# Optimization experiments

Measured on AMD Instinct MI355X. Metric: run time of the kernel, lower is better.

Reference implementation:

```python
import jax, jax.numpy as jnp
import numpy as np

DIM = 768
H = 12
D = DIM // H  # head_dim = 64
SCALE = D ** -0.5


def _split_heads(x):
    # [b, n, h*d] -> [b, h, n, d]
    b, n, _ = x.shape
    return x.reshape(b, n, H, D).transpose(0, 2, 1, 3)


def setup_inputs() -> dict:
    key = jax.random.key(0)
    ks = jax.random.split(key, 16)
    B, NQ, NKV = 2, 2048, 2048
    w_init = lambda k: jax.random.normal(k, (DIM, DIM), dtype=jnp.float32) * 0.02
    return {
        "words": jax.random.normal(ks[0], (B, NQ, DIM), dtype=jnp.float32),
        "position_words": jax.random.normal(ks[1], (B, NQ, DIM), dtype=jnp.float32),
        "conscious_words": jax.random.normal(ks[2], (B, NQ, DIM), dtype=jnp.float32),
        "cross_kv": jax.random.normal(ks[3], (B, NKV, DIM), dtype=jnp.float32),
        "position_cross": jax.random.normal(ks[4], (B, NKV, DIM), dtype=jnp.float32),
        "Wq_w": w_init(ks[5]), "Wk_w": w_init(ks[6]), "Wv_w": w_init(ks[7]),
        "Wq_p": w_init(ks[8]), "Wk_p": w_init(ks[9]),
        "Wq_c": w_init(ks[10]), "Wk_c": w_init(ks[11]),
        "latent_k": jax.random.normal(ks[12], (DIM,), dtype=jnp.float32),
        "Wo": w_init(ks[13]),
        "bo": jnp.zeros((DIM,), dtype=jnp.float32),
    }


def reference(words, position_words, conscious_words, cross_kv, position_cross,
              Wq_w, Wk_w, Wv_w, Wq_p, Wk_p, Wq_c, Wk_c, latent_k, Wo, bo):
    # Queries from three sources. Sum of the 9 pairwise QK^T scores equals
    # (sum of Qs) @ (sum of Ks)^T by bilinearity of matmul (same math as source).
    q = _split_heads(words @ Wq_w) + _split_heads(position_words @ Wq_p) \
        + _split_heads(conscious_words @ Wq_c)        # [b,h,nq,d]
    # latent conscious key: same vector for every kv position
    kc = (latent_k @ Wk_c).reshape(H, D)              # [h,d]
    k = _split_heads(cross_kv @ Wk_w) + _split_heads(position_cross @ Wk_p) \
        + kc[None, :, None, :]                        # [b,h,nkv,d]
    v = _split_heads(cross_kv @ Wv_w)                 # [b,h,nkv,d]

    score = jnp.einsum('bhid,bhjd->bhij', q, k) * SCALE  # [b,h,nq,nkv]
    attn = jax.nn.softmax(score, axis=-1)
    out = jnp.einsum('bhij,bhjd->bhid', attn, v)      # [b,h,nq,d]
    b, _, nq, _ = out.shape
    out = out.transpose(0, 2, 1, 3).reshape(b, nq, H * D)
    return out @ Wo + bo
```

## Files before the change

### kernel.cpp

```cpp
#include <hip/hip_runtime.h>
#include <math.h>

#define DIM  768
#define NH   12
#define HD   64
#define NQ   2048
#define NKV  2048
#define QSC_LOG2E 0.18033688011112042f

typedef short bf16x8  __attribute__((ext_vector_type(8)));
typedef float f32x4   __attribute__((ext_vector_type(4)));
typedef float f32x16  __attribute__((ext_vector_type(16)));

__device__ __forceinline__ unsigned short f2bf(float f) {
    unsigned u = __float_as_uint(f);
    unsigned r = (u + 0x7FFFu + ((u >> 16) & 1u)) >> 16;
    return (unsigned short)r;
}
__device__ __forceinline__ float bf2f(unsigned short u) {
    return __uint_as_float(((unsigned)u) << 16);
}

__device__ __forceinline__ unsigned cvtpk_bf16(float a, float b) {
    unsigned r;
    asm("v_cvt_pk_bf16_f32 %0, %1, %2" : "=v"(r) : "v"(a), "v"(b));
    return r;
}

__device__ __forceinline__ void plswap(unsigned& a, unsigned& b) {
    asm("v_permlane32_swap_b32 %0, %1" : "+v"(a), "+v"(b));
}

__device__ __forceinline__ float vexp2f(float x) {
#if __has_builtin(__builtin_amdgcn_exp2f)
    return __builtin_amdgcn_exp2f(x);
#else
    float r;
    asm("v_exp_f32 %0, %1\ns_nop 0" : "=v"(r) : "v"(x));
    return r;
#endif
}

__device__ __forceinline__ void ld_lds16(void* lds, const void* g) {
    __builtin_amdgcn_global_load_lds(
        (const __attribute__((address_space(1))) unsigned int*)g,
        (__attribute__((address_space(3))) unsigned int*)lds, 16, 0, 0);
}

__device__ __forceinline__ f32x16 z16() {
    f32x16 r;
    #pragma unroll
    for (int e = 0; e < 16; ++e) r[e] = 0.f;
    return r;
}

union PB16 { unsigned u[4]; bf16x8 v; };

__global__ __launch_bounds__(256)
void prep_kernel(const float* __restrict__ w0, const float* __restrict__ w1,
                 const float* __restrict__ w2, const float* __restrict__ w3,
                 const float* __restrict__ w4, const float* __restrict__ w5,
                 const float* __restrict__ w6, unsigned short* __restrict__ wt,
                 const float* __restrict__ latent, const float* __restrict__ Wkc,
                 float* __restrict__ kc) {
    __shared__ float t[32][33];
    int bid = blockIdx.x;
    if (bid < 4032) {
        int iz = bid / 576, rem = bid - iz * 576;
        int iy = rem / 24, ix = rem - iy * 24;
        const float* Ws[7] = {w0, w1, w2, w3, w4, w5, w6};
        const float* W = Ws[iz];
        unsigned short* D = wt + (size_t)iz * (768 * 768);
        int r0 = iy * 32, c0 = ix * 32;
        int tx = threadIdx.x & 31, ty = threadIdx.x >> 5;
        #pragma unroll
        for (int yy = 0; yy < 4; ++yy)
            t[ty * 4 + yy][tx] = W[(size_t)(r0 + ty * 4 + yy) * 768 + c0 + tx];
        __syncthreads();
        #pragma unroll
        for (int yy = 0; yy < 4; ++yy)
            D[(size_t)(c0 + ty * 4 + yy) * 768 + r0 + tx] = f2bf(t[tx][ty * 4 + yy]);
    } else {
        int jb = bid - 4032;
        float (&red)[16][17] = *reinterpret_cast<float(*)[16][17]>(&t[0][0]);
        int tx = threadIdx.x & 15, ty = threadIdx.x >> 4;
        int j = jb * 16 + tx;
        float acc = 0.f;
        for (int i = ty * 48; i < ty * 48 + 48; ++i)
            acc += latent[i] * Wkc[i * DIM + j];
        red[ty][tx] = acc;
        __syncthreads();
        if (ty == 0) {
            float s = 0.f;
            #pragma unroll
            for (int k = 0; k < 16; ++k) s += red[k][tx];
            kc[j] = s;
        }
    }
}

struct QCfg {
    const float* A0; const float* A1; const float* A2;
    const unsigned short* B0; const unsigned short* B1; const unsigned short* B2;
    const float* bias; float scale; void* out; int npair; int mode;
};

__global__ __launch_bounds__(256, 3)
void gemm_qvk(QCfg c0, QCfg c1, QCfg c2) {
    __shared__ unsigned short As[2][64 * 64];
    __shared__ unsigned short Bs[2][128 * 64];
    const int tid = threadIdx.x;
    const int w = tid >> 6, l = tid & 63, g = l >> 4, r16 = l & 15;

    int p = blockIdx.x;
    int xcd = p & 7, s = p >> 3;
    int bx = s % 6, gg = s / 6;
    int gidx = gg * 8 + xcd;
    int by = gidx & 63, z = gidx >> 6;
    const int n0 = bx * 128, m0 = by * 64;

    QCfg c = (z == 0) ? c0 : (z == 1) ? c1 : c2;
    const float* Alist[3] = {c.A0, c.A1, c.A2};
    const unsigned short* Blist[3] = {c.B0, c.B1, c.B2};

    const int ar = tid >> 2, ac = (tid & 3) * 16;
    const int aswz = (ar & 7) << 4;

    f32x4 acc[4][2];
    #pragma unroll
    for (int i = 0; i < 4; ++i)
        #pragma unroll
        for (int j = 0; j < 2; ++j) acc[i][j] = (f32x4){0.f, 0.f, 0.f, 0.f};

    const int NSTEPS = c.npair * 12;
    int pnA = 0, knA = 0;
    int pnB = 0, knB = 0;
    float4 xa0, xa1, xa2, xa3;
    float4 ya0, ya1, ya2, ya3;

#define ALOADX { const float* _ap = Alist[pnA] + (size_t)(m0 + ar) * 768 + knA + ac; \
    xa0 = *(const float4*)_ap;       xa1 = *(const float4*)(_ap + 4); \
    xa2 = *(const float4*)(_ap + 8); xa3 = *(const float4*)(_ap + 12); \
    knA += 64; if (knA == 768) { knA = 0; ++pnA; } }
#define ALOADY { const float* _ap = Alist[pnA] + (size_t)(m0 + ar) * 768 + knA + ac; \
    ya0 = *(const float4*)_ap;       ya1 = *(const float4*)(_ap + 4); \
    ya2 = *(const float4*)(_ap + 8); ya3 = *(const float4*)(_ap + 12); \
    knA += 64; if (knA == 768) { knA = 0; ++pnA; } }
#define AWR(BUFI, v0, v1, v2, v3) { uint4 u0_, u1_; \
    u0_.x = cvtpk_bf16(v0.x, v0.y); u0_.y = cvtpk_bf16(v0.z, v0.w); \
    u0_.z = cvtpk_bf16(v1.x, v1.y); u0_.w = cvtpk_bf16(v1.z, v1.w); \
    u1_.x = cvtpk_bf16(v2.x, v2.y); u1_.y = cvtpk_bf16(v2.z, v2.w); \
    u1_.z = cvtpk_bf16(v3.x, v3.y); u1_.w = cvtpk_bf16(v3.z, v3.w); \
    char* _dst = (char*)As[BUFI] + ar * 128; \
    *(uint4*)(_dst + ((2 * ac) ^ aswz)) = u0_; \
    *(uint4*)(_dst + ((2 * ac + 16) ^ aswz)) = u1_; }
#define BSTG(BUFI) { const unsigned short* _bp = Blist[pnB]; \
    _Pragma("unroll") \
    for (int is = 0; is < 4; ++is) { \
        int u = is * 256 + tid, r = u >> 3, cc2 = u & 7; \
        int col = ((cc2 ^ (r & 7)) << 3); \
        ld_lds16((char*)Bs[BUFI] + is * 4096 + w * 1024, \
                 _bp + (size_t)(n0 + r) * 768 + knB + col); } \
    knB += 64; if (knB == 768) { knB = 0; ++pnB; } }
#define COMPUTE(BUFI) { const char* Ab = (const char*)As[BUFI]; \
    const char* Bb = (const char*)Bs[BUFI]; \
    _Pragma("unroll") \
    for (int kk = 0; kk < 2; ++kk) { \
        bf16x8 af[4], bf[2]; \
        _Pragma("unroll") \
        for (int i = 0; i < 4; ++i) { int row = i * 16 + r16; \
            af[i] = *(const bf16x8*)(Ab + row * 128 + ((kk * 64 + g * 16) ^ ((row & 7) << 4))); } \
        _Pragma("unroll") \
        for (int j = 0; j < 2; ++j) { int row = w * 32 + j * 16 + r16; \
            bf[j] = *(const bf16x8*)(Bb + row * 128 + ((kk * 64 + g * 16) ^ ((row & 7) << 4))); } \
        _Pragma("unroll") \
        for (int i = 0; i < 4; ++i) \
            _Pragma("unroll") \
            for (int j = 0; j < 2; ++j) \
                acc[i][j] = __builtin_amdgcn_mfma_f32_16x16x32_bf16( \
                    af[i], bf[j], acc[i][j], 0, 0, 0); } }
#define WAITV4 asm volatile("s_waitcnt vmcnt(4)" ::: "memory")
#define WAITV0 asm volatile("s_waitcnt vmcnt(0)" ::: "memory")
#define WAITL0 asm volatile("s_waitcnt lgkmcnt(0)" ::: "memory")

    ALOADX;
    BSTG(0);
    ALOADY;
    AWR(0, xa0, xa1, xa2, xa3);
    WAITV4; WAITL0;
    __builtin_amdgcn_s_barrier();

    const int P = NSTEPS >> 1;
    #pragma unroll 1
    for (int it = 0; it < P; ++it) {
        const int st = it * 2;
        BSTG(1);
        const bool a2 = (st + 2 < NSTEPS);
        if (a2) ALOADX;
        COMPUTE(0);
        AWR(1, ya0, ya1, ya2, ya3);
        if (a2) { WAITV4; } else { WAITV0; }
        WAITL0;
        __builtin_amdgcn_s_barrier();
        const bool b2 = (st + 2 < NSTEPS);
        const bool a3 = (st + 3 < NSTEPS);
        if (b2) BSTG(0);
        if (a3) ALOADY;
        COMPUTE(1);
        if (b2) {
            AWR(0, xa0, xa1, xa2, xa3);
            if (a3) { WAITV4; } else { WAITV0; }
            WAITL0;
            __builtin_amdgcn_s_barrier();
        }
    }
#undef ALOADX
#undef ALOADY
#undef AWR
#undef BSTG
#undef COMPUTE
#undef WAITV4
#undef WAITV0
#undef WAITL0

    const int mode = c.mode;
    #pragma unroll
    for (int i = 0; i < 4; ++i) {
        #pragma unroll
        for (int j = 0; j < 2; ++j) {
            int col = n0 + w * 32 + j * 16 + r16;
            float bv = (mode == 0 && c.bias) ? c.bias[col] : 0.f;
            #pragma unroll
            for (int rr = 0; rr < 4; ++rr) {
                int row = m0 + i * 16 + g * 4 + rr;
                float v = acc[i][j][rr];
                if (mode == 2) v *= c.scale;
                v += bv;
                if (mode == 3) {
                    int bb = row >> 11, q = row & 2047;
                    ((unsigned short*)c.out)[(size_t)(bb * 768 + col) * 2048 + q] = f2bf(v);
                } else {
                    ((unsigned short*)c.out)[(size_t)row * 768 + col] = f2bf(v);
                }
            }
        }
    }
}

__global__ __launch_bounds__(256)
void gemm_out(const unsigned short* __restrict__ A,
              const unsigned short* __restrict__ B,
              const float* __restrict__ bias, float* __restrict__ Cout) {
    __shared__ unsigned short As[2][64 * 64];
    __shared__ unsigned short Bs[2][128 * 64];
    const int tid = threadIdx.x;
    const int w = tid >> 6, l = tid & 63, g = l >> 4, r16 = l & 15;

    int o_lin = blockIdx.x;
    int wl = (o_lin & 7) * 48 + (o_lin >> 3);
    int bx = wl % 6, by = wl / 6;
    const int n0 = bx * 128, m0 = by * 64;

    f32x4 acc[4][2];
    #pragma unroll
    for (int i = 0; i < 4; ++i)
        #pragma unroll
        for (int j = 0; j < 2; ++j) acc[i][j] = (f32x4){0.f, 0.f, 0.f, 0.f};

#define GSTAGE(BUFI, K0) { \
    _Pragma("unroll") \
    for (int is = 0; is < 2; ++is) { \
        int u = is * 256 + tid, r = u >> 3, cc = u & 7; \
        int col = ((cc ^ (r & 7)) << 3); \
        ld_lds16((char*)As[BUFI] + is * 4096 + w * 1024, \
                 A + (size_t)(m0 + r) * 768 + (K0) + col); } \
    _Pragma("unroll") \
    for (int is = 0; is < 4; ++is) { \
        int u = is * 256 + tid, r = u >> 3, cc = u & 7; \
        int col = ((cc ^ (r & 7)) << 3); \
        ld_lds16((char*)Bs[BUFI] + is * 4096 + w * 1024, \
                 B + (size_t)(n0 + r) * 768 + (K0) + col); } }

    GSTAGE(0, 0);
    __syncthreads();

    #pragma unroll 1
    for (int st = 0; st < 12; ++st) {
        int cur = st & 1;
        if (st + 1 < 12) GSTAGE(cur ^ 1, (st + 1) * 64);
        const char* Ab = (const char*)As[cur];
        const char* Bb = (const char*)Bs[cur];
        #pragma unroll
        for (int kk = 0; kk < 2; ++kk) {
            bf16x8 af[4], bf[2];
            #pragma unroll
            for (int i = 0; i < 4; ++i) {
                int row = i * 16 + r16;
                af[i] = *(const bf16x8*)(Ab + row * 128 +
                          ((kk * 64 + g * 16) ^ ((row & 7) << 4)));
            }
            #pragma unroll
            for (int j = 0; j < 2; ++j) {
                int row = w * 32 + j * 16 + r16;
                bf[j] = *(const bf16x8*)(Bb + row * 128 +
                          ((kk * 64 + g * 16) ^ ((row & 7) << 4)));
            }
            #pragma unroll
            for (int i = 0; i < 4; ++i)
                #pragma unroll
                for (int j = 0; j < 2; ++j)
                    acc[i][j] = __builtin_amdgcn_mfma_f32_16x16x32_bf16(
                        af[i], bf[j], acc[i][j], 0, 0, 0);
        }
        __syncthreads();
    }
#undef GSTAGE

    #pragma unroll
    for (int i = 0; i < 4; ++i) {
        #pragma unroll
        for (int j = 0; j < 2; ++j) {
            int col = n0 + w * 32 + j * 16 + r16;
            float bv = bias[col];
            #pragma unroll
            for (int rr = 0; rr < 4; ++rr) {
                int row = m0 + i * 16 + g * 4 + rr;
                Cout[(size_t)row * 768 + col] = acc[i][j][rr] + bv;
            }
        }
    }
}

__global__ __launch_bounds__(256)
void flash2(const unsigned short* __restrict__ Qb,
            const unsigned short* __restrict__ Kb,
            const unsigned short* __restrict__ Vt,
            unsigned short* __restrict__ P0, unsigned short* __restrict__ P1,
            unsigned short* __restrict__ P2, unsigned short* __restrict__ P3,
            float2* __restrict__ ML) {
    __shared__ unsigned short KV[2][2][4096];
    const int tid = threadIdx.x;
    const int w = tid >> 6, l = tid & 63, lo = l & 31, hi = l >> 5;

    int p = blockIdx.x + 64 * blockIdx.y;
    int xcd = p & 7, s = p >> 3;
    int gg = s >> 6, inner = s & 63;
    int bh = gg * 8 + xcd;
    int qi = inner >> 2, part = inner & 3;
    int b = bh / NH, h = bh % NH;
    int q0 = qi * 128;
    int kvbase = part * 512;

    bf16x8 qf[4];
    {
        const unsigned short* Qrow =
            Qb + (size_t)(b * NQ + q0 + w * 32 + lo) * DIM + h * HD + hi * 8;
        #pragma unroll
        for (int kc = 0; kc < 4; ++kc) qf[kc] = *(const bf16x8*)(Qrow + kc * 16);
    }

    f32x16 o0 = z16(), o1 = z16();
    float m = -3.0e38f, lsum = 0.f;

    const unsigned short* Kbase = Kb + (size_t)(b * NKV) * DIM + h * HD;
    const unsigned short* Vbase = Vt + ((size_t)b * DIM + h * HD) * NKV;

#define FSTAGE(BUFI, T0) { \
    _Pragma("unroll") \
    for (int is = 0; is < 2; ++is) { \
        int u = is * 256 + tid, r = u >> 3, cc = u & 7; \
        int col = ((cc ^ (r & 7)) << 3); \
        ld_lds16((char*)KV[BUFI][0] + is * 4096 + w * 1024, \
                 Kbase + (size_t)((T0) + r) * 768 + col); \
        ld_lds16((char*)KV[BUFI][1] + is * 4096 + w * 1024, \
                 Vbase + (size_t)r * 2048 + (T0) + col); } }

    FSTAGE(0, kvbase);
    __syncthreads();

    #pragma unroll 1
    for (int t = 0; t < 8; ++t) {
        int cur = t & 1;
        if (t < 7) FSTAGE(cur ^ 1, kvbase + (t + 1) * 64);

        const char* Kp = (const char*)KV[cur][0];
        const char* Vp = (const char*)KV[cur][1];

        f32x16 s0 = z16(), s1 = z16();
        __builtin_amdgcn_s_setprio(1);
        #pragma unroll
        for (int kc = 0; kc < 4; ++kc) {
            int r0 = lo, r1 = 32 + lo;
            bf16x8 k0 = *(const bf16x8*)(Kp + r0 * 128 +
                          ((kc * 32 + hi * 16) ^ ((r0 & 7) << 4)));
            bf16x8 k1 = *(const bf16x8*)(Kp + r1 * 128 +
                          ((kc * 32 + hi * 16) ^ ((r1 & 7) << 4)));
            s0 = __builtin_amdgcn_mfma_f32_32x32x16_bf16(k0, qf[kc], s0, 0, 0, 0);
            s1 = __builtin_amdgcn_mfma_f32_32x32x16_bf16(k1, qf[kc], s1, 0, 0, 0);
        }
        __builtin_amdgcn_s_setprio(0);

        float a8[8];
        #pragma unroll
        for (int e = 0; e < 8; ++e)
            a8[e] = fmaxf(fmaxf(fmaxf(s0[e], s0[e + 8]), s1[e]), s1[e + 8]);
        float pm = fmaxf(fmaxf(fmaxf(a8[0], a8[1]), fmaxf(a8[2], a8[3])),
                         fmaxf(fmaxf(a8[4], a8[5]), fmaxf(a8[6], a8[7])));
        pm = fmaxf(pm, __shfl_xor(pm, 32));

        if (__any(pm > m + 10.f)) {
            float mn = fmaxf(m, pm);
            float sc = vexp2f(m - mn);
            lsum *= sc;
            #pragma unroll
            for (int e = 0; e < 16; ++e) { o0[e] *= sc; o1[e] *= sc; }
            m = mn;
        }

        #pragma unroll
        for (int e = 0; e < 16; ++e) {
            s0[e] = vexp2f(s0[e] - m);
            s1[e] = vexp2f(s1[e] - m);
        }

        float b8[8];
        #pragma unroll
        for (int e = 0; e < 8; ++e)
            b8[e] = (s0[e] + s0[e + 8]) + (s1[e] + s1[e + 8]);
        float rs = ((b8[0] + b8[1]) + (b8[2] + b8[3])) +
                   ((b8[4] + b8[5]) + (b8[6] + b8[7]));
        rs += __shfl_xor(rs, 32);
        lsum += rs;

        PB16 pb[4];
        #pragma unroll
        for (int cc = 0; cc < 2; ++cc) {
            unsigned a0 = cvtpk_bf16(s0[cc * 8 + 0], s0[cc * 8 + 1]);
            unsigned a1 = cvtpk_bf16(s0[cc * 8 + 2], s0[cc * 8 + 3]);
            unsigned b0 = cvtpk_bf16(s0[cc * 8 + 4], s0[cc * 8 + 5]);
            unsigned b1 = cvtpk_bf16(s0[cc * 8 + 6], s0[cc * 8 + 7]);
            plswap(a0, b0);
            plswap(a1, b1);
            pb[cc].u[0] = a0; pb[cc].u[1] = a1; pb[cc].u[2] = b0; pb[cc].u[3] = b1;
            unsigned c0 = cvtpk_bf16(s1[cc * 8 + 0], s1[cc * 8 + 1]);
            unsigned c1 = cvtpk_bf16(s1[cc * 8 + 2], s1[cc * 8 + 3]);
            unsigned d0 = cvtpk_bf16(s1[cc * 8 + 4], s1[cc * 8 + 5]);
            unsigned d1 = cvtpk_bf16(s1[cc * 8 + 6], s1[cc * 8 + 7]);
            plswap(c0, d0);
            plswap(c1, d1);
            pb[2 + cc].u[0] = c0; pb[2 + cc].u[1] = c1;
            pb[2 + cc].u[2] = d0; pb[2 + cc].u[3] = d1;
        }

        __builtin_amdgcn_s_setprio(1);
        #pragma unroll
        for (int c = 0; c < 4; ++c) {
            int r0 = lo, r1 = 32 + lo;
            bf16x8 v0 = *(const bf16x8*)(Vp + r0 * 128 +
                          ((c * 32 + hi * 16) ^ ((r0 & 7) << 4)));
            bf16x8 v1 = *(const bf16x8*)(Vp + r1 * 128 +
                          ((c * 32 + hi * 16) ^ ((r1 & 7) << 4)));
            o0 = __builtin_amdgcn_mfma_f32_32x32x16_bf16(v0, pb[c].v, o0, 0, 0, 0);
            o1 = __builtin_amdgcn_mfma_f32_32x32x16_bf16(v1, pb[c].v, o1, 0, 0, 0);
        }
        __builtin_amdgcn_s_setprio(0);
        __syncthreads();
    }
#undef FSTAGE

    unsigned short* Pp = (part == 0) ? P0 : (part == 1) ? P1 : (part == 2) ? P2 : P3;
    const int q = q0 + w * 32 + lo;
    unsigned short* Op = Pp + ((size_t)bh * 2048 + q) * 64;
    #pragma unroll
    for (int grp = 0; grp < 4; ++grp) {
        int r0 = grp * 4;
        int d0 = grp * 8 + 4 * hi;
        uint2 v0, v1;
        v0.x = cvtpk_bf16(o0[r0 + 0], o0[r0 + 1]);
        v0.y = cvtpk_bf16(o0[r0 + 2], o0[r0 + 3]);
        *(uint2*)(Op + d0) = v0;
        v1.x = cvtpk_bf16(o1[r0 + 0], o1[r0 + 1]);
        v1.y = cvtpk_bf16(o1[r0 + 2], o1[r0 + 3]);
        *(uint2*)(Op + 32 + d0) = v1;
    }
    if (hi == 0)
        ML[(size_t)(part * 24 + bh) * 2048 + q] = make_float2(m, lsum);
}

__global__ __launch_bounds__(256)
void combine4(const unsigned short* __restrict__ P0, const unsigned short* __restrict__ P1,
              const unsigned short* __restrict__ P2, const unsigned short* __restrict__ P3,
              const float2* __restrict__ ML, unsigned short* __restrict__ AO) {
    int bh = blockIdx.y;
    int idx = blockIdx.x * 256 + threadIdx.x;
    int q = idx >> 1, dh = (idx & 1) * 32;

    float2 u0 = ML[(size_t)(0 * 24 + bh) * 2048 + q];
    float2 u1 = ML[(size_t)(1 * 24 + bh) * 2048 + q];
    float2 u2 = ML[(size_t)(2 * 24 + bh) * 2048 + q];
    float2 u3 = ML[(size_t)(3 * 24 + bh) * 2048 + q];
    float M = fmaxf(fmaxf(u0.x, u1.x), fmaxf(u2.x, u3.x));
    float w0 = vexp2f(u0.x - M), w1 = vexp2f(u1.x - M);
    float w2 = vexp2f(u2.x - M), w3 = vexp2f(u3.x - M);
    float inv = 1.f / (w0 * u0.y + w1 * u1.y + w2 * u2.y + w3 * u3.y);
    w0 *= inv; w1 *= inv; w2 *= inv; w3 *= inv;

    size_t off = ((size_t)bh * 2048 + q) * 64 + dh;
    float acc[32];
    #pragma unroll
    for (int e = 0; e < 32; ++e) acc[e] = 0.f;
    const unsigned short* Ps[4] = {P0, P1, P2, P3};
    float ws[4] = {w0, w1, w2, w3};
    #pragma unroll
    for (int pp = 0; pp < 4; ++pp) {
        const unsigned short* src = Ps[pp] + off;
        float wv = ws[pp];
        #pragma unroll
        for (int c = 0; c < 4; ++c) {
            uint4 vv = *(const uint4*)(src + c * 8);
            unsigned uu[4] = {vv.x, vv.y, vv.z, vv.w};
            #pragma unroll
            for (int e = 0; e < 4; ++e) {
                acc[c * 8 + e * 2 + 0] += wv * bf2f((unsigned short)(uu[e] & 0xFFFF));
                acc[c * 8 + e * 2 + 1] += wv * bf2f((unsigned short)(uu[e] >> 16));
            }
        }
    }
    int b = bh / NH, h = bh % NH;
    unsigned short* dst = AO + ((size_t)(b * 2048 + q)) * DIM + h * HD + dh;
    #pragma unroll
    for (int c = 0; c < 4; ++c) {
        uint4 ov;
        ov.x = cvtpk_bf16(acc[c * 8 + 0], acc[c * 8 + 1]);
        ov.y = cvtpk_bf16(acc[c * 8 + 2], acc[c * 8 + 3]);
        ov.z = cvtpk_bf16(acc[c * 8 + 4], acc[c * 8 + 5]);
        ov.w = cvtpk_bf16(acc[c * 8 + 6], acc[c * 8 + 7]);
        *(uint4*)(dst + c * 8) = ov;
    }
}

extern "C" void kernel_launch(void* const* d_in, const int* in_sizes, int n_in,
                              void* d_out, int out_size, void* d_ws, size_t ws_size,
                              hipStream_t stream) {
    const float* words   = (const float*)d_in[0];
    const float* posw    = (const float*)d_in[1];
    const float* consc   = (const float*)d_in[2];
    const float* cross   = (const float*)d_in[3];
    const float* pcross  = (const float*)d_in[4];
    const float* Wq_w    = (const float*)d_in[5];
    const float* Wk_w    = (const float*)d_in[6];
    const float* Wv_w    = (const float*)d_in[7];
    const float* Wq_p    = (const float*)d_in[8];
    const float* Wk_p    = (const float*)d_in[9];
    const float* Wq_c    = (const float*)d_in[10];
    const float* Wk_c    = (const float*)d_in[11];
    const float* latentk = (const float*)d_in[12];
    const float* Wo      = (const float*)d_in[13];
    const float* bo      = (const float*)d_in[14];

    char* arena = (char*)d_ws;
    const size_t WTE = 768 * 768;
    unsigned short* WT = (unsigned short*)(arena);
    unsigned short* QB = (unsigned short*)(arena + 8257536);
    unsigned short* VT = (unsigned short*)(arena + 14548992);
    unsigned short* KB = (unsigned short*)(arena + 20840448);
    unsigned short* P0 = (unsigned short*)(arena + 27131904);
    unsigned short* P1 = (unsigned short*)(arena + 33423360);
    unsigned short* P2 = (unsigned short*)(arena + 39714816);
    unsigned short* P3 = (unsigned short*)(arena);
    float2* ML         = (float2*)(arena + 46006272);
    float* KCV         = (float*)(arena + 47579136);

    prep_kernel<<<dim3(4080), dim3(256), 0, stream>>>(
        Wq_w, Wq_p, Wq_c, Wk_w, Wk_p, Wv_w, Wo, WT, latentk, Wk_c, KCV);

    QCfg cq = { words, posw, consc,
                WT + 0 * WTE, WT + 1 * WTE, WT + 2 * WTE,
                nullptr, QSC_LOG2E, QB, 3, 2 };
    QCfg cv = { cross, nullptr, nullptr,
                WT + 5 * WTE, nullptr, nullptr,
                nullptr, 1.f, VT, 1, 3 };
    QCfg ck = { cross, pcross, nullptr,
                WT + 3 * WTE, WT + 4 * WTE, nullptr,
                KCV, 1.f, KB, 2, 0 };
    gemm_qvk<<<dim3(1152), dim3(256), 0, stream>>>(cq, cv, ck);

    flash2<<<dim3(64, 24), dim3(256), 0, stream>>>(QB, KB, VT, P0, P1, P2, P3, ML);

    combine4<<<dim3(16, 24), dim3(256), 0, stream>>>(P0, P1, P2, P3, ML, QB);

    gemm_out<<<dim3(384), dim3(256), 0, stream>>>(QB, WT + 6 * WTE, bo, (float*)d_out);
}
```

Baseline: 142.1 us.

## Deepen QKV projection GEMM pipeline to triple-buffered LDS stages

Converts the projection GEMM's double-buffered LDS pipeline into a three-stage ring. A and B tiles are prefetched two steps ahead, with vmcnt waits retuned for the deeper queue, so global load latency is hidden behind more compute. The cost is more LDS per block (three buffers) and more live A registers. The launch bound minimum of 3 blocks per SM is also dropped, which can reduce occupancy.

```diff
diff --git a/kernel.cpp b/kernel.cpp
--- a/kernel.cpp
+++ b/kernel.cpp
@@ -105,10 +105,10 @@
     const float* bias; float scale; void* out; int npair; int mode;
 };
 
-__global__ __launch_bounds__(256, 3)
+__global__ __launch_bounds__(256)
 void gemm_qvk(QCfg c0, QCfg c1, QCfg c2) {
-    __shared__ unsigned short As[2][64 * 64];
-    __shared__ unsigned short Bs[2][128 * 64];
+    __shared__ unsigned short As[3][64 * 64];
+    __shared__ unsigned short Bs[3][128 * 64];
     const int tid = threadIdx.x;
     const int w = tid >> 6, l = tid & 63, g = l >> 4, r16 = l & 15;
 
@@ -137,14 +137,12 @@
     int pnB = 0, knB = 0;
     float4 xa0, xa1, xa2, xa3;
     float4 ya0, ya1, ya2, ya3;
-
-#define ALOADX { const float* _ap = Alist[pnA] + (size_t)(m0 + ar) * 768 + knA + ac; \
-    xa0 = *(const float4*)_ap;       xa1 = *(const float4*)(_ap + 4); \
-    xa2 = *(const float4*)(_ap + 8); xa3 = *(const float4*)(_ap + 12); \
-    knA += 64; if (knA == 768) { knA = 0; ++pnA; } }
-#define ALOADY { const float* _ap = Alist[pnA] + (size_t)(m0 + ar) * 768 + knA + ac; \
-    ya0 = *(const float4*)_ap;       ya1 = *(const float4*)(_ap + 4); \
-    ya2 = *(const float4*)(_ap + 8); ya3 = *(const float4*)(_ap + 12); \
+    float4 za0, za1, za2, za3;
+
+#define ALOAD(p0, p1, p2, p3) { \
+    const float* _ap = Alist[pnA] + (size_t)(m0 + ar) * 768 + knA + ac; \
+    p0 = *(const float4*)_ap;       p1 = *(const float4*)(_ap + 4); \
+    p2 = *(const float4*)(_ap + 8); p3 = *(const float4*)(_ap + 12); \
     knA += 64; if (knA == 768) { knA = 0; ++pnA; } }
 #define AWR(BUFI, v0, v1, v2, v3) { uint4 u0_, u1_; \
     u0_.x = cvtpk_bf16(v0.x, v0.y); u0_.y = cvtpk_bf16(v0.z, v0.w); \
@@ -179,49 +177,59 @@
             for (int j = 0; j < 2; ++j) \
                 acc[i][j] = __builtin_amdgcn_mfma_f32_16x16x32_bf16( \
                     af[i], bf[j], acc[i][j], 0, 0, 0); } }
+#define WAITV8 asm volatile("s_waitcnt vmcnt(8)" ::: "memory")
 #define WAITV4 asm volatile("s_waitcnt vmcnt(4)" ::: "memory")
 #define WAITV0 asm volatile("s_waitcnt vmcnt(0)" ::: "memory")
 #define WAITL0 asm volatile("s_waitcnt lgkmcnt(0)" ::: "memory")
-
-    ALOADX;
+#define BARRIER __builtin_amdgcn_s_barrier()
+
+    ALOAD(xa0, xa1, xa2, xa3);
+    ALOAD(ya0, ya1, ya2, ya3);
+    ALOAD(za0, za1, za2, za3);
     BSTG(0);
-    ALOADY;
+    BSTG(1);
     AWR(0, xa0, xa1, xa2, xa3);
-    WAITV4; WAITL0;
-    __builtin_amdgcn_s_barrier();
-
-    const int P = NSTEPS >> 1;
+    WAITV4;
+    WAITL0;
+    BARRIER;
+
+    const int NIT = NSTEPS / 3;
     #pragma unroll 1
-    for (int it = 0; it < P; ++it) {
-        const int st = it * 2;
-        BSTG(1);
-        const bool a2 = (st + 2 < NSTEPS);
-        if (a2) ALOADX;
+    for (int it = 0; it < NIT; ++it) {
+        const bool lastit = (it == NIT - 1);
+        if (!lastit) ALOAD(xa0, xa1, xa2, xa3);
+        BSTG(2);
         COMPUTE(0);
         AWR(1, ya0, ya1, ya2, ya3);
-        if (a2) { WAITV4; } else { WAITV0; }
+        if (!lastit) { WAITV8; } else { WAITV4; }
         WAITL0;
-        __builtin_amdgcn_s_barrier();
-        const bool b2 = (st + 2 < NSTEPS);
-        const bool a3 = (st + 3 < NSTEPS);
-        if (b2) BSTG(0);
-        if (a3) ALOADY;
+        BARRIER;
+        if (!lastit) { ALOAD(ya0, ya1, ya2, ya3); BSTG(0); }
         COMPUTE(1);
-        if (b2) {
+        AWR(2, za0, za1, za2, za3);
+        if (!lastit) { WAITV8; } else { WAITV0; }
+        WAITL0;
+        BARRIER;
+        if (!lastit) {
+            ALOAD(za0, za1, za2, za3); BSTG(1);
+            COMPUTE(2);
             AWR(0, xa0, xa1, xa2, xa3);
-            if (a3) { WAITV4; } else { WAITV0; }
+            WAITV8;
             WAITL0;
-            __builtin_amdgcn_s_barrier();
-        }
-    }
-#undef ALOADX
-#undef ALOADY
+            BARRIER;
+        } else {
+            COMPUTE(2);
+        }
+    }
+#undef ALOAD
 #undef AWR
 #undef BSTG
 #undef COMPUTE
+#undef WAITV8
 #undef WAITV4
 #undef WAITV0
 #undef WAITL0
+#undef BARRIER
 
     const int mode = c.mode;
     #pragma unroll
```

Result: slower. 150.1 us (+5.6%).

## Fuse split-KV combine into flash kernel via last-block atomic counter

Applied to the files above, without the earlier changes.

Removes the separate combine4 kernel. Each flash2 block now bumps a per-(head, query-tile) atomic counter after writing its partial output and its max/sum pair. The fourth block to finish merges the four partials into the attention output buffer. This saves one kernel launch and one dependency boundary, at the cost of a memset of the counters, thread fences, and extra serial tail work in the last-arriving block.

```diff
diff --git a/kernel.cpp b/kernel.cpp
--- a/kernel.cpp
+++ b/kernel.cpp
@@ -337,8 +337,10 @@
             const unsigned short* __restrict__ Vt,
             unsigned short* __restrict__ P0, unsigned short* __restrict__ P1,
             unsigned short* __restrict__ P2, unsigned short* __restrict__ P3,
-            float2* __restrict__ ML) {
+            float2* __restrict__ ML, unsigned int* __restrict__ cnt,
+            unsigned short* __restrict__ AO) {
     __shared__ unsigned short KV[2][2][4096];
+    __shared__ int lastFlag;
     const int tid = threadIdx.x;
     const int w = tid >> 6, l = tid & 63, lo = l & 31, hi = l >> 5;
 
@@ -485,57 +487,60 @@
     }
     if (hi == 0)
         ML[(size_t)(part * 24 + bh) * 2048 + q] = make_float2(m, lsum);
-}
-
-__global__ __launch_bounds__(256)
-void combine4(const unsigned short* __restrict__ P0, const unsigned short* __restrict__ P1,
-              const unsigned short* __restrict__ P2, const unsigned short* __restrict__ P3,
-              const float2* __restrict__ ML, unsigned short* __restrict__ AO) {
-    int bh = blockIdx.y;
-    int idx = blockIdx.x * 256 + threadIdx.x;
-    int q = idx >> 1, dh = (idx & 1) * 32;
-
-    float2 u0 = ML[(size_t)(0 * 24 + bh) * 2048 + q];
-    float2 u1 = ML[(size_t)(1 * 24 + bh) * 2048 + q];
-    float2 u2 = ML[(size_t)(2 * 24 + bh) * 2048 + q];
-    float2 u3 = ML[(size_t)(3 * 24 + bh) * 2048 + q];
-    float M = fmaxf(fmaxf(u0.x, u1.x), fmaxf(u2.x, u3.x));
-    float w0 = vexp2f(u0.x - M), w1 = vexp2f(u1.x - M);
-    float w2 = vexp2f(u2.x - M), w3 = vexp2f(u3.x - M);
-    float inv = 1.f / (w0 * u0.y + w1 * u1.y + w2 * u2.y + w3 * u3.y);
-    w0 *= inv; w1 *= inv; w2 *= inv; w3 *= inv;
-
-    size_t off = ((size_t)bh * 2048 + q) * 64 + dh;
-    float acc[32];
-    #pragma unroll
-    for (int e = 0; e < 32; ++e) acc[e] = 0.f;
-    const unsigned short* Ps[4] = {P0, P1, P2, P3};
-    float ws[4] = {w0, w1, w2, w3};
-    #pragma unroll
-    for (int pp = 0; pp < 4; ++pp) {
-        const unsigned short* src = Ps[pp] + off;
-        float wv = ws[pp];
+
+    __threadfence();
+    __syncthreads();
+    if (tid == 0) {
+        unsigned old = atomicAdd(&cnt[bh * 16 + qi], 1u);
+        lastFlag = (old == 3u);
+    }
+    __syncthreads();
+    if (lastFlag) {
+        __threadfence();
+        int cq = q0 + (tid >> 1);
+        int dh = (tid & 1) * 32;
+
+        float2 u0 = ML[(size_t)(0 * 24 + bh) * 2048 + cq];
+        float2 u1 = ML[(size_t)(1 * 24 + bh) * 2048 + cq];
+        float2 u2 = ML[(size_t)(2 * 24 + bh) * 2048 + cq];
+        float2 u3 = ML[(size_t)(3 * 24 + bh) * 2048 + cq];
+        float M = fmaxf(fmaxf(u0.x, u1.x), fmaxf(u2.x, u3.x));
+        float w0 = vexp2f(u0.x - M), w1 = vexp2f(u1.x - M);
+        float w2 = vexp2f(u2.x - M), w3 = vexp2f(u3.x - M);
+        float inv = 1.f / (w0 * u0.y + w1 * u1.y + w2 * u2.y + w3 * u3.y);
+        w0 *= inv; w1 *= inv; w2 *= inv; w3 *= inv;
+
+        size_t off = ((size_t)bh * 2048 + cq) * 64 + dh;
+        float acc[32];
+        #pragma unroll
+        for (int e = 0; e < 32; ++e) acc[e] = 0.f;
+        const unsigned short* Ps[4] = {P0, P1, P2, P3};
+        float ws[4] = {w0, w1, w2, w3};
+        #pragma unroll
+        for (int pp = 0; pp < 4; ++pp) {
+            const unsigned short* src = Ps[pp] + off;
+            float wv = ws[pp];
+            #pragma unroll
+            for (int c = 0; c < 4; ++c) {
+                uint4 vv = *(const uint4*)(src + c * 8);
+                unsigned uu[4] = {vv.x, vv.y, vv.z, vv.w};
+                #pragma unroll
+                for (int e = 0; e < 4; ++e) {
+                    acc[c * 8 + e * 2 + 0] += wv * bf2f((unsigned short)(uu[e] & 0xFFFF));
+                    acc[c * 8 + e * 2 + 1] += wv * bf2f((unsigned short)(uu[e] >> 16));
+                }
+            }
+        }
+        unsigned short* dst = AO + ((size_t)(b * 2048 + cq)) * DIM + h * HD + dh;
         #pragma unroll
         for (int c = 0; c < 4; ++c) {
-            uint4 vv = *(const uint4*)(src + c * 8);
-            unsigned uu[4] = {vv.x, vv.y, vv.z, vv.w};
-            #pragma unroll
-            for (int e = 0; e < 4; ++e) {
-                acc[c * 8 + e * 2 + 0] += wv * bf2f((unsigned short)(uu[e] & 0xFFFF));
-                acc[c * 8 + e * 2 + 1] += wv * bf2f((unsigned short)(uu[e] >> 16));
-            }
-        }
-    }
-    int b = bh / NH, h = bh % NH;
-    unsigned short* dst = AO + ((size_t)(b * 2048 + q)) * DIM + h * HD + dh;
-    #pragma unroll
-    for (int c = 0; c < 4; ++c) {
-        uint4 ov;
-        ov.x = cvtpk_bf16(acc[c * 8 + 0], acc[c * 8 + 1]);
-        ov.y = cvtpk_bf16(acc[c * 8 + 2], acc[c * 8 + 3]);
-        ov.z = cvtpk_bf16(acc[c * 8 + 4], acc[c * 8 + 5]);
-        ov.w = cvtpk_bf16(acc[c * 8 + 6], acc[c * 8 + 7]);
-        *(uint4*)(dst + c * 8) = ov;
+            uint4 ov;
+            ov.x = cvtpk_bf16(acc[c * 8 + 0], acc[c * 8 + 1]);
+            ov.y = cvtpk_bf16(acc[c * 8 + 2], acc[c * 8 + 3]);
+            ov.z = cvtpk_bf16(acc[c * 8 + 4], acc[c * 8 + 5]);
+            ov.w = cvtpk_bf16(acc[c * 8 + 6], acc[c * 8 + 7]);
+            *(uint4*)(dst + c * 8) = ov;
+        }
     }
 }
 
@@ -570,6 +575,9 @@
     unsigned short* P3 = (unsigned short*)(arena);
     float2* ML         = (float2*)(arena + 46006272);
     float* KCV         = (float*)(arena + 47579136);
+    unsigned int* CNT  = (unsigned int*)(arena + 47582208);
+
+    hipMemsetAsync(CNT, 0, 384 * sizeof(unsigned int), stream);
 
     prep_kernel<<<dim3(4080), dim3(256), 0, stream>>>(
         Wq_w, Wq_p, Wq_c, Wk_w, Wk_p, Wv_w, Wo, WT, latentk, Wk_c, KCV);
@@ -585,9 +593,8 @@
                 KCV, 1.f, KB, 2, 0 };
     gemm_qvk<<<dim3(1152), dim3(256), 0, stream>>>(cq, cv, ck);
 
-    flash2<<<dim3(64, 24), dim3(256), 0, stream>>>(QB, KB, VT, P0, P1, P2, P3, ML);
-
-    combine4<<<dim3(16, 24), dim3(256), 0, stream>>>(P0, P1, P2, P3, ML, QB);
+    flash2<<<dim3(64, 24), dim3(256), 0, stream>>>(
+        QB, KB, VT, P0, P1, P2, P3, ML, CNT, QB);
 
     gemm_out<<<dim3(384), dim3(256), 0, stream>>>(QB, WT + 6 * WTE, bo, (float*)d_out);
 }
```

Result: slower. 397.6 us (+179.8%).
